# Optimization experiments

Measured on AMD Instinct MI355X. Metric: run time of the kernel, lower is better.

## Reference

```python
import jax, jax.numpy as jnp
import numpy as np

B, T, H = 64, 1024, 256

def _lstm_cell(x, h, c, Wih, Whh, bih, bhh):
    # torch gate order: i, f, g, o
    gates = x @ Wih.T + h @ Whh.T + bih + bhh  # [B, 4H]
    i, f, g, o = jnp.split(gates, 4, axis=-1)
    i = jax.nn.sigmoid(i)
    f = jax.nn.sigmoid(f)
    g = jnp.tanh(g)
    o = jax.nn.sigmoid(o)
    c_new = f * c + i * g
    h_new = o * jnp.tanh(c_new)
    return h_new, c_new


def setup_inputs() -> dict:
    key = jax.random.key(0)
    ks = jax.random.split(key, 11)
    s = 1.0 / np.sqrt(H)
    def u(k, shape):
        return jax.random.uniform(k, shape, jnp.float32, -s, s)
    return {
        "x": jax.random.normal(ks[0], (B, T, 1), jnp.float32),
        "enc_Wih": u(ks[1], (4 * H, 1)),
        "enc_Whh": u(ks[2], (4 * H, H)),
        "enc_bih": u(ks[3], (4 * H,)),
        "enc_bhh": u(ks[4], (4 * H,)),
        "dec_Wih": u(ks[5], (4 * H, 1)),
        "dec_Whh": u(ks[6], (4 * H, H)),
        "dec_bih": u(ks[7], (4 * H,)),
        "dec_bhh": u(ks[8], (4 * H,)),
        "lin_W": u(ks[9], (1, 2 * H)),
        "lin_b": u(ks[10], (1,)),
    }


def reference(x, enc_Wih, enc_Whh, enc_bih, enc_bhh,
              dec_Wih, dec_Whh, dec_bih, dec_bhh, lin_W, lin_b):
    b = x.shape[0]
    h = x.shape[2] * 0  # placeholder, not used
    hidden = enc_Whh.shape[1]

    x_t = jnp.transpose(x, (1, 0, 2))  # [T, B, 1]

    # ---- encoder: single-layer LSTM over time ----
    def enc_step(carry, xt):
        hh, cc = carry
        hh, cc = _lstm_cell(xt, hh, cc, enc_Wih, enc_Whh, enc_bih, enc_bhh)
        return (hh, cc), hh
    h0 = jnp.zeros((b, hidden), x.dtype)
    (h_last, _), enc_seq = jax.lax.scan(enc_step, (h0, h0), x_t)
    encoder_states = jnp.transpose(enc_seq, (1, 0, 2))  # [B, T, H]

    # ---- decoder: LSTMCell + dot attention + linear, per step ----
    def dec_step(carry, xt):
        hx, cx = carry
        hx, cx = _lstm_cell(xt, hx, cx, dec_Wih, dec_Whh, dec_bih, dec_bhh)
        scores = jnp.einsum('bth,bh->bt', encoder_states, hx)  # dot attention
        attn = jax.nn.softmax(scores, axis=1)
        ctx = jnp.einsum('bt,bth->bh', attn, encoder_states)
        updated = jnp.concatenate([ctx, hx], axis=1)  # [B, 2H]
        res = updated @ lin_W.T + lin_b  # [B, 1]
        return (hx, cx), res

    cx0 = jnp.zeros_like(h_last)
    _, outs = jax.lax.scan(dec_step, (h_last, cx0), x_t)  # [T, B, 1]
    return jnp.transpose(outs, (1, 0, 2))  # [B, T, 1]
```

## Files before the change

kernel.cpp:

```cpp
#include <hip/hip_runtime.h>
#include <math.h>

#define HD 256
#define GD 1024
#define TT 1024
#define BB 64
#define NT 512

__device__ __forceinline__ float sig_(float x)  { return 1.f / (1.f + __expf(-x)); }
__device__ __forceinline__ float tanh_(float x) { return 1.f - 2.f / (1.f + __expf(2.f * x)); }

__global__ __launch_bounds__(256) void prep_kernel(
    const float* __restrict__ eW, const float* __restrict__ eb1, const float* __restrict__ eb2,
    const float* __restrict__ dW, const float* __restrict__ db1, const float* __restrict__ db2,
    float* __restrict__ WTe, float* __restrict__ WTd,
    float* __restrict__ be, float* __restrict__ bd,
    unsigned long long* __restrict__ ex_all)
{
    int idx = blockIdx.x * 256 + threadIdx.x;
    if (idx < GD * HD) {
        int j = idx / HD, k = idx % HD;
        WTe[k * GD + j] = eW[idx];
        WTd[k * GD + j] = dW[idx];
    }
    if (idx < GD) {
        be[idx] = eb1[idx] + eb2[idx];
        bd[idx] = db1[idx] + db2[idx];
    }
    if (idx < 4 * BB * 2 * 256) ex_all[idx] = 0ULL;
}

__global__ __launch_bounds__(NT, 2) void lstm_scan_coop(
    const float* __restrict__ x,
    const float* __restrict__ Wih,
    const float* __restrict__ bias,
    const float* __restrict__ WT,
    const float* __restrict__ h_init,
    float* __restrict__ states,
    unsigned long long* __restrict__ exf,
    unsigned long long* __restrict__ exs)
{
    const int b   = blockIdx.x & 63;
    const int q   = blockIdx.x >> 6;
    const int tid = threadIdx.x;
    const int s   = tid & 3;
    const int jj  = tid >> 2;
    const int gate = jj >> 5;
    const int kk0  = (jj & 31) * 2;
    const int r0   = gate * 64 + kk0;
    const int jg0  = gate * 256 + q * 64 + kk0;

    __shared__ float h_rep[4][264];
    __shared__ float act_s[256];
    __shared__ float x_s[TT];

    float4 w0[16], w1[16];
    {
        const float* basek = WT + (size_t)(s * 64) * GD;
        #pragma unroll
        for (int i = 0; i < 16; ++i) {
            const float* p0 = basek + (size_t)(4 * i) * GD + jg0;
            w0[i] = make_float4(p0[0], p0[GD], p0[2 * GD], p0[3 * GD]);
            const float* p1 = p0 + 1;
            w1[i] = make_float4(p1[0], p1[GD], p1[2 * GD], p1[3 * GD]);
        }
    }
    const float wih0 = Wih[jg0], wih1 = Wih[jg0 + 1];
    const float bj0  = bias[jg0], bj1  = bias[jg0 + 1];

    for (int i = tid; i < TT; i += NT) x_s[i] = x[b * TT + i];
    if (tid < 256) {
        float hv = h_init ? h_init[((size_t)b * TT + (TT - 1)) * HD + tid] : 0.f;
        h_rep[tid >> 6][tid & 63] = hv;
    }
    float c = 0.f;
    bool fast_ok = true;
    __syncthreads();

    for (int t = 0; t < TT; ++t) {
        const float xt = x_s[t];
        float a0p, a1p, a0q = 0.f, a1q = 0.f;
        if (s == 0) { a0p = fmaf(xt, wih0, bj0); a1p = fmaf(xt, wih1, bj1); }
        else        { a0p = 0.f;                 a1p = 0.f; }
        const float4* h4 = (const float4*)(&h_rep[s][0]);
        #pragma unroll
        for (int i = 0; i < 8; ++i) {
            float4 hv = h4[i];
            a0p = fmaf(hv.x, w0[i].x, a0p); a0p = fmaf(hv.y, w0[i].y, a0p);
            a0p = fmaf(hv.z, w0[i].z, a0p); a0p = fmaf(hv.w, w0[i].w, a0p);
            a1p = fmaf(hv.x, w1[i].x, a1p); a1p = fmaf(hv.y, w1[i].y, a1p);
            a1p = fmaf(hv.z, w1[i].z, a1p); a1p = fmaf(hv.w, w1[i].w, a1p);
        }
        #pragma unroll
        for (int i = 8; i < 16; ++i) {
            float4 hv = h4[i];
            a0q = fmaf(hv.x, w0[i].x, a0q); a0q = fmaf(hv.y, w0[i].y, a0q);
            a0q = fmaf(hv.z, w0[i].z, a0q); a0q = fmaf(hv.w, w0[i].w, a0q);
            a1q = fmaf(hv.x, w1[i].x, a1q); a1q = fmaf(hv.y, w1[i].y, a1q);
            a1q = fmaf(hv.z, w1[i].z, a1q); a1q = fmaf(hv.w, w1[i].w, a1q);
        }
        float a0 = a0p + a0q;
        float a1 = a1p + a1q;
        a0 += __shfl_xor(a0, 1); a0 += __shfl_xor(a0, 2);
        a1 += __shfl_xor(a1, 1); a1 += __shfl_xor(a1, 2);
        if (s == 0) {
            float2 av;
            av.x = (gate == 2) ? tanh_(a0) : sig_(a0);
            av.y = (gate == 2) ? tanh_(a1) : sig_(a1);
            *(float2*)(&act_s[r0]) = av;
        }
        __syncthreads();

        const size_t pbase = ((size_t)b * 2 + (t & 1)) * 256;
        if (tid < 256) {
            const int dq = tid >> 6, dk = tid & 63;
            unsigned long long* fs = exf + pbase + tid;
            unsigned long long* ss = exs + pbase + tid;
            if (dq == q) {
                float gi = act_s[dk], gf = act_s[64 + dk], gg = act_s[128 + dk], go = act_s[192 + dk];
                c = fmaf(gf, c, gi * gg);
                float h = go * tanh_(c);
                unsigned long long pk = ((unsigned long long)(unsigned)(t + 1) << 32)
                                      | (unsigned long long)__float_as_uint(h);
                asm volatile("global_store_dwordx2 %0, %1, off sc0"
                             :: "v"(fs), "v"(pk) : "memory");
                __hip_atomic_store(ss, pk, __ATOMIC_RELAXED, __HIP_MEMORY_SCOPE_AGENT);
                h_rep[q][dk] = h;
                states[((size_t)(b * TT + t)) * HD + tid] = h;
            } else {
                const unsigned want = (unsigned)(t + 1);
                unsigned long long v;
                if (fast_ok) {
                    int spins = 0;
                    for (;;) {
                        asm volatile("global_load_dwordx2 %0, %1, off sc0\n\ts_waitcnt vmcnt(0)"
                                     : "=v"(v) : "v"(fs) : "memory");
                        if ((unsigned)(v >> 32) == want) break;
                        if (++spins > 96) { fast_ok = false; break; }
                    }
                }
                if (!fast_ok) {
                    do {
                        v = __hip_atomic_load(ss, __ATOMIC_RELAXED, __HIP_MEMORY_SCOPE_AGENT);
                    } while ((unsigned)(v >> 32) != want);
                }
                h_rep[dq][dk] = __uint_as_float((unsigned)v);
            }
        }
        __syncthreads();
    }
}

__global__ __launch_bounds__(256) void proj_kernel(
    const float* __restrict__ enc_states, const float* __restrict__ dec_hs,
    const float* __restrict__ linW, float* __restrict__ ew, float* __restrict__ hw)
{
    const int lane = threadIdx.x & 63;
    const int wid  = blockIdx.x * 4 + (threadIdx.x >> 6);
    const int nw   = gridDim.x * 4;
    const float4 w1 = ((const float4*)linW)[lane];
    const float4 w2 = ((const float4*)(linW + HD))[lane];
    for (int o = wid; o < BB * TT; o += nw) {
        float4 v1 = ((const float4*)(enc_states + (size_t)o * HD))[lane];
        float4 v2 = ((const float4*)(dec_hs     + (size_t)o * HD))[lane];
        float s1 = v1.x * w1.x + v1.y * w1.y + v1.z * w1.z + v1.w * w1.w;
        float s2 = v2.x * w2.x + v2.y * w2.y + v2.z * w2.z + v2.w * w2.w;
        #pragma unroll
        for (int m = 1; m < 64; m <<= 1) {
            s1 += __shfl_xor(s1, m);
            s2 += __shfl_xor(s2, m);
        }
        if (lane == 0) { ew[o] = s1; hw[o] = s2; }
    }
}

#define TD2  32
#define TEC2 256
#define KC2  32
__global__ __launch_bounds__(256) void attn_kernel(
    const float* __restrict__ enc_states,
    const float* __restrict__ dec_hs,
    const float* __restrict__ ew, const float* __restrict__ hw,
    const float* __restrict__ lin_b,
    float* __restrict__ out)
{
    const int b   = blockIdx.y;
    const int td0 = blockIdx.x * TD2;
    const int tid = threadIdx.x;
    const int tdt = tid >> 5;
    const int tet = tid & 31;

    __shared__ float Hx[HD][TD2 + 4];
    __shared__ float E[KC2][TEC2];

    {
        const int td = tid >> 3;
        const int kc = (tid & 7) * 32;
        const float* src = dec_hs + ((size_t)b * TT + td0 + td) * HD + kc;
        #pragma unroll
        for (int qq = 0; qq < 8; ++qq) {
            float4 v = ((const float4*)(src + qq * 4))[0];
            Hx[kc + qq * 4 + 0][td] = v.x;
            Hx[kc + qq * 4 + 1][td] = v.y;
            Hx[kc + qq * 4 + 2][td] = v.z;
            Hx[kc + qq * 4 + 3][td] = v.w;
        }
    }

    float M[4]  = {-1e30f, -1e30f, -1e30f, -1e30f};
    float Nm[4] = {0.f, 0.f, 0.f, 0.f};
    float Dn[4] = {0.f, 0.f, 0.f, 0.f};

    for (int tc = 0; tc < TT / TEC2; ++tc) {
        const int te0 = tc * TEC2;
        float S[4][8] = {{0.f}};
        for (int kc = 0; kc < HD / KC2; ++kc) {
            const int k0 = kc * KC2;
            __syncthreads();
            {
                const float* src = enc_states + ((size_t)b * TT + te0 + tid) * HD + k0;
                #pragma unroll
                for (int qq = 0; qq < 8; ++qq) {
                    float4 v = ((const float4*)(src + qq * 4))[0];
                    E[qq * 4 + 0][tid] = v.x;
                    E[qq * 4 + 1][tid] = v.y;
                    E[qq * 4 + 2][tid] = v.z;
                    E[qq * 4 + 3][tid] = v.w;
                }
            }
            __syncthreads();
            #pragma unroll 4
            for (int k = 0; k < KC2; ++k) {
                const float4 hx4 = *(const float4*)(&Hx[k0 + k][tdt * 4]);
                #pragma unroll
                for (int i = 0; i < 8; ++i) {
                    const float e = E[k][tet + 32 * i];
                    S[0][i] = fmaf(hx4.x, e, S[0][i]);
                    S[1][i] = fmaf(hx4.y, e, S[1][i]);
                    S[2][i] = fmaf(hx4.z, e, S[2][i]);
                    S[3][i] = fmaf(hx4.w, e, S[3][i]);
                }
            }
        }
        float ewv[8];
        #pragma unroll
        for (int i = 0; i < 8; ++i) ewv[i] = ew[(size_t)b * TT + te0 + tet + 32 * i];
        #pragma unroll
        for (int r = 0; r < 4; ++r) {
            float cm = S[r][0];
            #pragma unroll
            for (int i = 1; i < 8; ++i) cm = fmaxf(cm, S[r][i]);
            #pragma unroll
            for (int m = 1; m < 32; m <<= 1) cm = fmaxf(cm, __shfl_xor(cm, m));
            const float newM  = fmaxf(M[r], cm);
            const float scale = __expf(M[r] - newM);
            float nl = 0.f, dl = 0.f;
            #pragma unroll
            for (int i = 0; i < 8; ++i) {
                const float p = __expf(S[r][i] - newM);
                dl += p;
                nl = fmaf(p, ewv[i], nl);
            }
            #pragma unroll
            for (int m = 1; m < 32; m <<= 1) {
                nl += __shfl_xor(nl, m);
                dl += __shfl_xor(dl, m);
            }
            Nm[r] = Nm[r] * scale + nl;
            Dn[r] = Dn[r] * scale + dl;
            M[r]  = newM;
        }
    }

    if (tet == 0) {
        const float lb = lin_b[0];
        #pragma unroll
        for (int r = 0; r < 4; ++r) {
            const int td = td0 + tdt * 4 + r;
            out[(size_t)b * TT + td] = Nm[r] / Dn[r] + hw[(size_t)b * TT + td] + lb;
        }
    }
}

extern "C" void kernel_launch(void* const* d_in, const int* in_sizes, int n_in,
                              void* d_out, int out_size, void* d_ws, size_t ws_size,
                              hipStream_t stream)
{
    const float* x    = (const float*)d_in[0];
    const float* eWih = (const float*)d_in[1];
    const float* eWhh = (const float*)d_in[2];
    const float* ebih = (const float*)d_in[3];
    const float* ebhh = (const float*)d_in[4];
    const float* dWih = (const float*)d_in[5];
    const float* dWhh = (const float*)d_in[6];
    const float* dbih = (const float*)d_in[7];
    const float* dbhh = (const float*)d_in[8];
    const float* linW = (const float*)d_in[9];
    const float* linb = (const float*)d_in[10];
    float* out = (float*)d_out;

    float* p = (float*)d_ws;
    float* WTe = p;        p += (size_t)GD * HD;
    float* WTd = p;        p += (size_t)GD * HD;
    float* be  = p;        p += GD;
    float* bd  = p;        p += GD;
    float* enc_states = p; p += (size_t)BB * TT * HD;
    float* dec_hs = p;     p += (size_t)BB * TT * HD;
    float* ew = p;         p += (size_t)BB * TT;
    float* hw = p;         p += (size_t)BB * TT;
    unsigned long long* ex_base = (unsigned long long*)p;
    unsigned long long* exf_e = ex_base + 0 * (size_t)BB * 2 * 256;
    unsigned long long* exs_e = ex_base + 1 * (size_t)BB * 2 * 256;
    unsigned long long* exf_d = ex_base + 2 * (size_t)BB * 2 * 256;
    unsigned long long* exs_d = ex_base + 3 * (size_t)BB * 2 * 256;
    p += (size_t)4 * BB * 2 * 256 * 2;

    prep_kernel<<<(GD * HD + 255) / 256, 256, 0, stream>>>(
        eWhh, ebih, ebhh, dWhh, dbih, dbhh, WTe, WTd, be, bd, ex_base);

    {
        const float* hi = nullptr;
        void* args[] = {(void*)&x, (void*)&eWih, (void*)&be, (void*)&WTe,
                        (void*)&hi, (void*)&enc_states, (void*)&exf_e, (void*)&exs_e};
        hipLaunchCooperativeKernel((void*)lstm_scan_coop, dim3(256), dim3(NT),
                                   args, 0, stream);
    }
    {
        const float* hi = enc_states;
        void* args[] = {(void*)&x, (void*)&dWih, (void*)&bd, (void*)&WTd,
                        (void*)&hi, (void*)&dec_hs, (void*)&exf_d, (void*)&exs_d};
        hipLaunchCooperativeKernel((void*)lstm_scan_coop, dim3(256), dim3(NT),
                                   args, 0, stream);
    }

    proj_kernel<<<256, 256, 0, stream>>>(enc_states, dec_hs, linW, ew, hw);
    attn_kernel<<<dim3(TT / TD2, BB), 256, 0, stream>>>(enc_states, dec_hs, ew, hw, linb, out);
}
```

Measured before the change: 3.941 ms.

## Assign LSTM batch/quarter work to blocks by XCD so exchange partners co-locate

Each block reads its hardware XCD id and publishes it. After a grid sync, blocks are remapped so that the four quarter-blocks of each batch element sit on the same XCD where possible, with spare blocks filling leftover slots. The fast same-XCD exchange path is enabled only when the producer's XCD matches. The aim is to keep the per-step h exchange inside one XCD's L2 and avoid cross-die traffic, at the cost of two extra grid syncs and some setup work.

```diff
diff --git a/kernel.cpp b/kernel.cpp
--- a/kernel.cpp
+++ b/kernel.cpp
@@ -1,5 +1,8 @@
 #include <hip/hip_runtime.h>
+#include <hip/hip_cooperative_groups.h>
 #include <math.h>
+
+namespace cg = cooperative_groups;
 
 #define HD 256
 #define GD 1024
@@ -38,11 +41,62 @@
     const float* __restrict__ h_init,
     float* __restrict__ states,
     unsigned long long* __restrict__ exf,
-    unsigned long long* __restrict__ exs)
-{
-    const int b   = blockIdx.x & 63;
-    const int q   = blockIdx.x >> 6;
+    unsigned long long* __restrict__ exs,
+    int* __restrict__ xcd_map,
+    int* __restrict__ asg)
+{
     const int tid = threadIdx.x;
+    cg::grid_group grid = cg::this_grid();
+
+    __shared__ int xm[256];
+
+    unsigned xcd_raw;
+    asm volatile("s_getreg_b32 %0, hwreg(20, 0, 32)" : "=s"(xcd_raw));
+    const int myx = (int)(xcd_raw & 7u);
+    if (tid == 0) xcd_map[blockIdx.x] = myx;
+    grid.sync();
+
+    for (int i = tid; i < 256; i += NT) xm[i] = xcd_map[i] & 7;
+    __syncthreads();
+
+    int my_c = -1, my_q = 0;
+    {
+        int cnt[8] = {0, 0, 0, 0, 0, 0, 0, 0};
+        int my_spare = -1, nsp = 0;
+        const int bid = (int)blockIdx.x;
+        for (int i = 0; i < 256; ++i) {
+            int xv = xm[i];
+            int r = cnt[xv]++;
+            if (r < 32) {
+                if (i == bid) { my_c = xv * 8 + (r >> 2); my_q = r & 3; }
+            } else {
+                if (i == bid) my_spare = nsp;
+                nsp++;
+            }
+        }
+        if (my_c < 0) {
+            int k = 0;
+            for (int xv = 0; xv < 8; ++xv) {
+                int start = cnt[xv] < 32 ? cnt[xv] : 32;
+                for (int slot = start; slot < 32; ++slot) {
+                    if (k == my_spare) { my_c = xv * 8 + (slot >> 2); my_q = slot & 3; }
+                    k++;
+                }
+            }
+        }
+    }
+    const int b = my_c;
+    const int q = my_q;
+
+    if (tid == 0)
+        __hip_atomic_store(&asg[b * 4 + q], myx, __ATOMIC_RELAXED, __HIP_MEMORY_SCOPE_AGENT);
+    grid.sync();
+
+    int prod_x[4];
+    #pragma unroll
+    for (int j = 0; j < 4; ++j)
+        prod_x[j] = __hip_atomic_load(&asg[b * 4 + j], __ATOMIC_RELAXED, __HIP_MEMORY_SCOPE_AGENT);
+
     const int s   = tid & 3;
     const int jj  = tid >> 2;
     const int gate = jj >> 5;
@@ -74,7 +128,7 @@
         h_rep[tid >> 6][tid & 63] = hv;
     }
     float c = 0.f;
-    bool fast_ok = true;
+    bool fast_ok = (tid < 256) ? (prod_x[tid >> 6] == myx) : false;
     __syncthreads();
 
     for (int t = 0; t < TT; ++t) {
@@ -314,6 +368,8 @@
     unsigned long long* exf_d = ex_base + 2 * (size_t)BB * 2 * 256;
     unsigned long long* exs_d = ex_base + 3 * (size_t)BB * 2 * 256;
     p += (size_t)4 * BB * 2 * 256 * 2;
+    int* xcd_map = (int*)p; p += 256;
+    int* asg     = (int*)p; p += BB * 4;
 
     prep_kernel<<<(GD * HD + 255) / 256, 256, 0, stream>>>(
         eWhh, ebih, ebhh, dWhh, dbih, dbhh, WTe, WTd, be, bd, ex_base);
@@ -321,14 +377,16 @@
     {
         const float* hi = nullptr;
         void* args[] = {(void*)&x, (void*)&eWih, (void*)&be, (void*)&WTe,
-                        (void*)&hi, (void*)&enc_states, (void*)&exf_e, (void*)&exs_e};
+                        (void*)&hi, (void*)&enc_states, (void*)&exf_e, (void*)&exs_e,
+                        (void*)&xcd_map, (void*)&asg};
         hipLaunchCooperativeKernel((void*)lstm_scan_coop, dim3(256), dim3(NT),
                                    args, 0, stream);
     }
     {
         const float* hi = enc_states;
         void* args[] = {(void*)&x, (void*)&dWih, (void*)&bd, (void*)&WTd,
-                        (void*)&hi, (void*)&dec_hs, (void*)&exf_d, (void*)&exs_d};
+                        (void*)&hi, (void*)&dec_hs, (void*)&exf_d, (void*)&exs_d,
+                        (void*)&xcd_map, (void*)&asg};
         hipLaunchCooperativeKernel((void*)lstm_scan_coop, dim3(256), dim3(NT),
                                    args, 0, stream);
     }
```

After: 4.132 ms. 4.8% more time.
